# Kernel tuning notes

Hardware: AMD Instinct MI355X
Metric: run time of the kernel (lower is better)

Reference implementation:

```python
import jax, jax.numpy as jnp
import numpy as np

NUM_HEADS = 16
NUM_KV_HEADS = 8
HEAD_DIM = 128
GATE_LOW_RANK = 16
GATE_NORMALIZER = 16.0
NORM_EPS = 1e-5
CHUNK = 64


def gla_chunk(q, k, v, g, chunk=CHUNK):
    """Chunkwise-parallel gated linear attention.
    q,k,v,g: [B,H,L,D]. Recurrence: S_t = diag(exp(g_t)) S_{t-1} + k_t^T v_t; o_t = q_t S_t.
    """
    B, H, L, D = q.shape
    n = L // chunk

    def rs(x):  # -> [n, B, H, C, D]
        return x.reshape(B, H, n, chunk, D).transpose(2, 0, 1, 3, 4)

    qc, kc, vc, gc = rs(q), rs(k), rs(v), rs(g)
    causal = jnp.tril(jnp.ones((chunk, chunk), dtype=bool))

    def step(S, inp):
        qt, kt, vt, gt = inp                      # [B,H,C,D]
        b = jnp.cumsum(gt, axis=-2)               # inclusive cumulative log-gates
        q_ = qt * jnp.exp(b)
        k_ = kt * jnp.exp(-b)
        # intra-chunk causal attention (diag included)
        A = jnp.einsum('bhid,bhjd->bhij', q_, k_)
        A = jnp.where(causal, A, 0.0)
        o = jnp.einsum('bhij,bhje->bhie', A, vt)
        # inter-chunk contribution from carried state
        o = o + jnp.einsum('bhid,bhde->bhie', q_, S)
        # state update to end of chunk
        k_end = kt * jnp.exp(b[..., -1:, :] - b)
        S_new = S * jnp.exp(b[..., -1, :])[..., None] + jnp.einsum('bhcd,bhce->bhde', k_end, vt)
        return S_new, o

    S0 = jnp.zeros((B, H, D, D), q.dtype)
    _, o = jax.lax.scan(step, S0, (qc, kc, vc, gc))
    return o.transpose(1, 2, 0, 3, 4).reshape(B, H, L, D)


def setup_inputs() -> dict:
    key = jax.random.key(0)
    ks = jax.random.split(key, 10)
    B, L, HID = 2, 2048, 2048
    KV = NUM_KV_HEADS * HEAD_DIM  # 1024
    w = 0.02
    return {
        'hidden_states': jax.random.normal(ks[0], (B, L, HID), jnp.float32),
        'Wq': jax.random.normal(ks[1], (HID, HID), jnp.float32) * w,
        'bq': jnp.zeros((HID,), jnp.float32),
        'Wk': jax.random.normal(ks[2], (HID, KV), jnp.float32) * w,
        'bk': jnp.zeros((KV,), jnp.float32),
        'Wv': jax.random.normal(ks[3], (HID, KV), jnp.float32) * w,
        'bv': jnp.zeros((KV,), jnp.float32),
        'Wg1': jax.random.normal(ks[4], (HID, GATE_LOW_RANK), jnp.float32) * w,
        'Wg2': jax.random.normal(ks[5], (GATE_LOW_RANK, KV), jnp.float32) * w,
        'bg2': jnp.zeros((KV,), jnp.float32),
        'g_norm_w': jnp.ones((HEAD_DIM,), jnp.float32),
        'Wo': jax.random.normal(ks[6], (HID, HID), jnp.float32) * w,
    }


def reference(hidden_states, Wq, bq, Wk, bk, Wv, bv, Wg1, Wg2, bg2, g_norm_w, Wo):
    B, L, HID = hidden_states.shape
    H, HKV, D = NUM_HEADS, NUM_KV_HEADS, HEAD_DIM
    n_rep = H // HKV

    q = jax.nn.relu(hidden_states @ Wq + bq)          # feature_map = relu
    k = jax.nn.relu(hidden_states @ Wk + bk)
    v = hidden_states @ Wv + bv
    gk = jax.nn.log_sigmoid((hidden_states @ Wg1) @ Wg2 + bg2) / GATE_NORMALIZER

    q = q.reshape(B, L, H, D).transpose(0, 2, 1, 3)    # [B,H,L,D]
    def to_heads(x):
        return x.reshape(B, L, HKV, D).transpose(0, 2, 1, 3)
    k, v, gk = to_heads(k), to_heads(v), to_heads(gk)  # [B,HKV,L,D]
    # GQA: repeat kv heads
    k = jnp.repeat(k, n_rep, axis=1)
    v = jnp.repeat(v, n_rep, axis=1)
    gk = jnp.repeat(gk, n_rep, axis=1)

    q = q * (D ** -0.5)                                # scale as in chunk_gla
    o = gla_chunk(q, k, v, gk)                         # [B,H,L,D]

    # per-head RMSNorm over head_dim
    o = o * jax.lax.rsqrt(jnp.mean(o * o, axis=-1, keepdims=True) + NORM_EPS) * g_norm_w
    o = o.transpose(0, 2, 1, 3).reshape(B, L, H * D)
    return o @ Wo
```

## Files before the change

### kernel.cpp

```cpp
#include <hip/hip_runtime.h>

typedef unsigned short u16;
typedef u16 u16x8 __attribute__((ext_vector_type(8)));
typedef u16 u16x4 __attribute__((ext_vector_type(4)));
typedef __bf16 bf16x8 __attribute__((ext_vector_type(8)));
typedef float f32x4 __attribute__((ext_vector_type(4)));

#define DEVI static __device__ __forceinline__

DEVI float b2f(u16 u){ union { unsigned u; float f; } c; c.u = ((unsigned)u) << 16; return c.f; }
DEVI u16 f2b(float f){ union { float f; unsigned u; } c; c.f = f;
  unsigned r = c.u + 0x7fffu + ((c.u >> 16) & 1u); return (u16)(r >> 16); }
DEVI void gload16(const void* g, void* l){
  __builtin_amdgcn_global_load_lds((const __attribute__((address_space(1))) void*)g,
                                   (__attribute__((address_space(3))) void*)l, 16, 0, 0);
}
DEVI f32x4 MFMA(bf16x8 a, bf16x8 b, f32x4 c){
  return __builtin_amdgcn_mfma_f32_16x16x32_bf16(a, b, c, 0, 0, 0);
}
#define WAITV(n) asm volatile("s_waitcnt vmcnt(" #n ")" ::: "memory")
#define WAITL0()  asm volatile("s_waitcnt lgkmcnt(0)" ::: "memory")

constexpr size_t OFF_HB  = 0;
constexpr size_t OFF_WCT = OFF_HB  + (size_t)4096*2048*2;
constexpr size_t OFF_WOT = OFF_WCT + (size_t)4224*2048*2;
constexpr size_t OFF_QKV = OFF_WOT + (size_t)2048*2048*2;
constexpr size_t OFF_G1  = OFF_QKV + (size_t)4096*4096*2;
constexpr size_t OFF_G   = OFF_G1  + (size_t)4096*16*4;
constexpr size_t OFF_EB  = OFF_G   + (size_t)4096*1024*4;
constexpr size_t OFF_KD  = OFF_EB  + (size_t)4096*1024*2;
constexpr size_t OFF_T   = OFF_KD  + (size_t)4096*1024*2;
constexpr size_t OFF_DV  = OFF_T   + (size_t)2*8*32*128*128*2;
constexpr size_t OFF_SP  = OFF_DV  + (size_t)2*8*32*128*4;
constexpr size_t OFF_ON  = OFF_SP  + (size_t)2*8*32*128*128*2;

__global__ __launch_bounds__(256) void k_conv_h(const float* __restrict__ h, u16* __restrict__ hb){
  int idx = blockIdx.x*256 + threadIdx.x, stride = gridDim.x*256;
  for (int i = idx; i < 4096*2048/4; i += stride){
    float4 v = ((const float4*)h)[i];
    u16x4 o; o[0]=f2b(v.x); o[1]=f2b(v.y); o[2]=f2b(v.z); o[3]=f2b(v.w);
    ((u16x4*)hb)[i] = o;
  }
}

__global__ __launch_bounds__(256) void k_transpose(const float* __restrict__ src, u16* __restrict__ dst,
                                                   int K, int N, int rowOff, int pitch){
  __shared__ float tile[64][65];
  int kb = blockIdx.y*64, nb = blockIdx.x*64;
  int t = threadIdx.x, x = t & 63, y0 = t >> 6;
#pragma unroll
  for (int i = 0; i < 16; i++){
    int y = y0 + i*4, k = kb + y, n = nb + x;
    tile[y][x] = (n < N) ? src[(size_t)k*N + n] : 0.f;
  }
  __syncthreads();
#pragma unroll
  for (int i = 0; i < 16; i++){
    int y = y0 + i*4, n = nb + y, k = kb + x;
    if (n < N) dst[(size_t)(rowOff + n)*pitch + k] = f2b(tile[x][y]);
  }
}

template<int BM, int MODE>
__global__ __launch_bounds__(512, 2) void gemm256(const u16* __restrict__ A, const u16* __restrict__ Bt,
                                                  u16* __restrict__ Cq, float* __restrict__ Cf,
                                                  const float* __restrict__ bq, const float* __restrict__ bk,
                                                  const float* __restrict__ bv){
  constexpr int NT = 64;
  constexpr int MI = BM/32;
  constexpr int ALOADS = BM/128;
  constexpr int NTN = (MODE==0) ? 16 : 8;
  __shared__ u16 sA[4*BM*32];
  __shared__ u16 sB[4*256*32];
  int id = blockIdx.x;
  int swz = (id & 7)*32 + (id >> 3);
  int mt = swz / NTN, nt = swz % NTN;
  int t = threadIdx.x, w = t >> 6, l = t & 63;
  int wr = w >> 2, wc = w & 3;
  int mRow0 = mt*BM, nCol0 = nt*256;
  const u16* srcA[ALOADS]; const u16* srcB[2];
#pragma unroll
  for (int i = 0; i < ALOADS; i++){
    int S = t + i*512, r = S>>2, g = (S&3) ^ ((r>>2)&3);
    srcA[i] = A + (size_t)(mRow0 + r)*2048 + g*8;
  }
#pragma unroll
  for (int i = 0; i < 2; i++){
    int S = t + i*512, r = S>>2, g = (S&3) ^ ((r>>2)&3);
    srcB[i] = Bt + (size_t)(nCol0 + r)*2048 + g*8;
  }
  auto ISSUE = [&](int T){
    int buf = T & 3;
    u16* dA = sA + buf*(BM*32);
    u16* dB = sB + buf*(256*32);
#pragma unroll
    for (int i = 0; i < ALOADS; i++) gload16(srcA[i] + T*32, dA + (i*512 + w*64)*8);
#pragma unroll
    for (int i = 0; i < 2; i++)      gload16(srcB[i] + T*32, dB + (i*512 + w*64)*8);
  };
  f32x4 acc[MI][4] = {};
  ISSUE(0); ISSUE(1); ISSUE(2);
  for (int T = 0; T < NT; ++T){
    if (T + 3 < NT) ISSUE(T + 3);
    if constexpr (BM == 256){
      if (T < NT-3)       WAITV(12);
      else if (T == NT-3) WAITV(8);
      else if (T == NT-2) WAITV(4);
      else                WAITV(0);
    } else {
      if (T < NT-3)       WAITV(9);
      else if (T == NT-3) WAITV(6);
      else if (T == NT-2) WAITV(3);
      else                WAITV(0);
    }
    __builtin_amdgcn_s_barrier();
    const u16* bufA = sA + (T&3)*(BM*32);
    const u16* bufB = sB + (T&3)*(256*32);
    bf16x8 bfr[4], afr[MI];
#pragma unroll
    for (int ni = 0; ni < 4; ni++){
      int r = wc*64 + ni*16 + (l&15);
      int p = (l>>4) ^ ((r>>2)&3);
      bfr[ni] = *(const bf16x8*)&bufB[(r*4 + p)*8];
    }
#pragma unroll
    for (int mi = 0; mi < MI; mi++){
      int r = wr*(BM/2) + mi*16 + (l&15);
      int p = (l>>4) ^ ((r>>2)&3);
      afr[mi] = *(const bf16x8*)&bufA[(r*4 + p)*8];
    }
    __builtin_amdgcn_s_setprio(1);
#pragma unroll
    for (int mi = 0; mi < MI; mi++)
#pragma unroll
      for (int ni = 0; ni < 4; ni++)
        acc[mi][ni] = MFMA(afr[mi], bfr[ni], acc[mi][ni]);
    __builtin_amdgcn_s_setprio(0);
    WAITL0();
    __builtin_amdgcn_s_barrier();
  }
  int iLoc = (l>>4)*4, jc = l & 15;
  if (MODE == 0){
#pragma unroll
    for (int ni = 0; ni < 4; ni++){
      int n0 = nCol0 + wc*64 + ni*16;
      int n = n0 + jc;
      int kind; float bias;
      if (n0 < 2048){ kind = 0; bias = bq[n]; }
      else if (n0 < 3072){ kind = 1; bias = bk[n - 2048]; }
      else { kind = 2; bias = bv[n - 3072]; }
#pragma unroll
      for (int mi = 0; mi < MI; mi++){
        int m = mRow0 + wr*(BM/2) + mi*16 + iLoc;
#pragma unroll
        for (int rr = 0; rr < 4; rr++){
          float x = acc[mi][ni][rr] + bias;
          int row = m + rr;
          if (kind == 0)      Cq[(size_t)row*4096 + n] = f2b(fmaxf(x, 0.f) * 0.08838834764831845f);
          else if (kind == 1) Cq[(size_t)row*4096 + n] = f2b(fmaxf(x, 0.f));
          else                Cq[(size_t)row*4096 + n] = f2b(x);
        }
      }
    }
  } else {
#pragma unroll
    for (int ni = 0; ni < 4; ni++){
      int n = nCol0 + wc*64 + ni*16 + jc;
#pragma unroll
      for (int mi = 0; mi < MI; mi++){
        int m = mRow0 + wr*(BM/2) + mi*16 + iLoc;
#pragma unroll
        for (int rr = 0; rr < 4; rr++) Cf[(size_t)(m+rr)*2048 + n] = acc[mi][ni][rr];
      }
    }
  }
}

__global__ __launch_bounds__(256) void k_g1(const u16* __restrict__ hb, const float* __restrict__ Wg1,
                                            float* __restrict__ G1){
  int t = threadIdx.x;
  int tok = blockIdx.x*16 + (t>>4), j = t & 15;
  const u16* hr = hb + (size_t)tok*2048;
  float s = 0.f;
  for (int k = 0; k < 2048; k += 8){
    u16x8 hv = *(const u16x8*)&hr[k];
#pragma unroll
    for (int u = 0; u < 8; u++) s += b2f(hv[u]) * Wg1[(k+u)*16 + j];
  }
  G1[(size_t)tok*16 + j] = s;
}

__global__ __launch_bounds__(256) void k_gates(const float* __restrict__ G1, const float* __restrict__ Wg2,
                                               const float* __restrict__ bg2, float* __restrict__ g){
  __shared__ float w2[16*1024];
  __shared__ float bb[1024];
  __shared__ float g1l[256];
  int t = threadIdx.x;
  for (int i = t; i < 4096; i += 256) ((float4*)w2)[i] = ((const float4*)Wg2)[i];
  ((float4*)bb)[t] = ((const float4*)bg2)[t];
  int tok0 = blockIdx.x*16;
  g1l[t] = G1[(size_t)tok0*16 + t];
  __syncthreads();
  int c0 = t*4;
  for (int tk = 0; tk < 16; tk++){
    float4 a = *(const float4*)&bb[c0];
#pragma unroll
    for (int r = 0; r < 16; r++){
      float gv = g1l[tk*16 + r];
      float4 wr = *(const float4*)&w2[r*1024 + c0];
      a.x += gv*wr.x; a.y += gv*wr.y; a.z += gv*wr.z; a.w += gv*wr.w;
    }
    float4 o;
    o.x = (fminf(a.x,0.f) - log1pf(expf(-fabsf(a.x)))) * 0.0625f;
    o.y = (fminf(a.y,0.f) - log1pf(expf(-fabsf(a.y)))) * 0.0625f;
    o.z = (fminf(a.z,0.f) - log1pf(expf(-fabsf(a.z)))) * 0.0625f;
    o.w = (fminf(a.w,0.f) - log1pf(expf(-fabsf(a.w)))) * 0.0625f;
    *(float4*)&g[(size_t)(tok0+tk)*1024 + c0] = o;
  }
}

__global__ __launch_bounds__(256) void k_phaseA(const float* __restrict__ g, const u16* __restrict__ QKV,
                                                u16* __restrict__ eb, u16* __restrict__ kd,
                                                u16* __restrict__ T, float* __restrict__ Dv){
  __shared__ float gb[64*128];
  __shared__ u16 keT[128*72];
  __shared__ u16 vT [128*72];
  int c = blockIdx.x, kvh = blockIdx.y, b = blockIdx.z;
  int t = threadIdx.x;
  int tok0 = b*2048 + c*64;
#pragma unroll
  for (int r = 0; r < 8; r++){
    int idx4 = r*256 + t;
    int i = idx4 >> 5, c4 = idx4 & 31;
    ((float4*)gb)[i*32 + c4] = *(const float4*)&g[(size_t)(tok0+i)*1024 + kvh*128 + c4*4];
  }
  __syncthreads();
  if (t < 128){
    float run = 0.f;
    for (int i = 0; i < 64; i++){ run += gb[i*128 + t]; gb[i*128 + t] = run; }
    Dv[((size_t)(b*8+kvh)*32 + c)*128 + t] = expf(run);
  }
  __syncthreads();
  int d0 = (t&15)*8;
  float blast[8];
#pragma unroll
  for (int j = 0; j < 8; j++) blast[j] = gb[63*128 + d0 + j];
#pragma unroll
  for (int r = 0; r < 4; r++){
    int i = (t>>4) + r*16;
    u16x8 kv_ = *(const u16x8*)&QKV[(size_t)(tok0+i)*4096 + 2048 + kvh*128 + d0];
    u16x8 vv  = *(const u16x8*)&QKV[(size_t)(tok0+i)*4096 + 3072 + kvh*128 + d0];
    u16x8 ebv, kdv;
#pragma unroll
    for (int j = 0; j < 8; j++){
      float bcur = gb[i*128 + d0 + j];
      float kf = b2f(kv_[j]);
      ebv[j] = f2b(expf(bcur));
      kdv[j] = f2b(kf * expf(-bcur));
      keT[(d0+j)*72 + i] = f2b(kf * expf(blast[j] - bcur));
      vT [(d0+j)*72 + i] = vv[j];
    }
    *(u16x8*)&eb[(size_t)(tok0+i)*1024 + kvh*128 + d0] = ebv;
    *(u16x8*)&kd[(size_t)(tok0+i)*1024 + kvh*128 + d0] = kdv;
  }
  __syncthreads();
  int w = t>>6, l = t&63;
  f32x4 acc[2][8] = {};
#pragma unroll
  for (int ks = 0; ks < 2; ks++){
    bf16x8 af[2];
#pragma unroll
    for (int ti = 0; ti < 2; ti++)
      af[ti] = *(const bf16x8*)&keT[(w*32 + ti*16 + (l&15))*72 + ks*32 + (l>>4)*8];
#pragma unroll
    for (int tj = 0; tj < 8; tj++){
      bf16x8 bf_ = *(const bf16x8*)&vT[(tj*16 + (l&15))*72 + ks*32 + (l>>4)*8];
#pragma unroll
      for (int ti = 0; ti < 2; ti++) acc[ti][tj] = MFMA(af[ti], bf_, acc[ti][tj]);
    }
  }
  size_t tbase = ((size_t)(b*8+kvh)*32 + c)*16384;
#pragma unroll
  for (int ti = 0; ti < 2; ti++)
#pragma unroll
    for (int tj = 0; tj < 8; tj++)
#pragma unroll
      for (int rr = 0; rr < 4; rr++){
        int d = w*32 + ti*16 + (l>>4)*4 + rr, e = tj*16 + (l&15);
        T[tbase + d*128 + e] = f2b(acc[ti][tj][rr]);
      }
}

__global__ __launch_bounds__(256) void k_phaseB(const u16* __restrict__ T, const float* __restrict__ Dv,
                                                u16* __restrict__ SP){
  __shared__ u16 sl[16*128];
  int es = blockIdx.x, kvh = blockIdx.y, b = blockIdx.z;
  int t = threadIdx.x;
  size_t bh = (size_t)(b*8 + kvh);
  float S[8] = {0,0,0,0,0,0,0,0};
  for (int c = 0; c < 32; c++){
#pragma unroll
    for (int r = 0; r < 8; r++){
      int idx = r*256 + t, d = idx>>4, el = idx&15;
      sl[el*128 + d] = f2b(S[r]);
    }
    __syncthreads();
    size_t spb = (bh*32 + c)*16384 + (size_t)es*2048;
    *(u16x8*)&SP[spb + t*8] = *(const u16x8*)&sl[t*8];
    size_t tb  = (bh*32 + c)*16384;
    size_t dvb = (bh*32 + c)*128;
#pragma unroll
    for (int r = 0; r < 8; r++){
      int idx = r*256 + t, d = idx>>4, el = idx&15;
      float tv = b2f(T[tb + d*128 + es*16 + el]);
      S[r] = S[r]*Dv[dvb + d] + tv;
    }
    __syncthreads();
  }
}

__global__ __launch_bounds__(256) void k_phaseC(const u16* __restrict__ QKV, const u16* __restrict__ eb,
                                                const u16* __restrict__ kd, const u16* __restrict__ SP,
                                                const float* __restrict__ gnw, u16* __restrict__ onrm){
  __shared__ u16 kl[64*128];
  __shared__ u16 sl[64*72];
  __shared__ u16 vT[128*72];
  int c = blockIdx.x, h = blockIdx.y, b = blockIdx.z;
  int kvh = h >> 1;
  int t = threadIdx.x, w = t>>6, l = t&63;
  int tok0 = b*2048 + c*64;
#pragma unroll
  for (int is = 0; is < 4; is++){
    int row = (t>>4) + is*16;
    int d0s = 8*((t&15) ^ (row&7));
    gload16(&kd[(size_t)(tok0+row)*1024 + kvh*128 + d0s], &kl[is*2048 + w*512]);
  }
  int d0v = (t&15)*8;
#pragma unroll
  for (int r = 0; r < 4; r++){
    int i = (t>>4) + r*16;
    u16x8 vv = *(const u16x8*)&QKV[(size_t)(tok0+i)*4096 + 3072 + kvh*128 + d0v];
#pragma unroll
    for (int jj = 0; jj < 8; jj++) vT[(d0v+jj)*72 + i] = vv[jj];
  }
  bf16x8 aq[4];
  {
    int i = w*16 + (l&15);
#pragma unroll
    for (int kt = 0; kt < 4; kt++){
      int dq = kt*32 + (l>>4)*8;
      u16x8 qv = *(const u16x8*)&QKV[(size_t)(tok0+i)*4096 + h*128 + dq];
      u16x8 ev = *(const u16x8*)&eb[(size_t)(tok0+i)*1024 + kvh*128 + dq];
      u16x8 o;
#pragma unroll
      for (int jj = 0; jj < 8; jj++) o[jj] = f2b(b2f(qv[jj]) * b2f(ev[jj]));
      aq[kt] = __builtin_bit_cast(bf16x8, o);
    }
  }
  __syncthreads();
  f32x4 accs[4] = {};
#pragma unroll
  for (int kt = 0; kt < 4; kt++){
#pragma unroll
    for (int jt = 0; jt < 4; jt++){
      int j = jt*16 + (l&15);
      int byte_ = j*256 + ((2*(kt*32 + (l>>4)*8)) ^ ((j&7)<<4));
      bf16x8 bk_ = *(const bf16x8*)((const char*)kl + byte_);
      accs[jt] = MFMA(aq[kt], bk_, accs[jt]);
    }
  }
#pragma unroll
  for (int jt = 0; jt < 4; jt++)
#pragma unroll
    for (int rr = 0; rr < 4; rr++){
      int i = w*16 + (l>>4)*4 + rr;
      int j = jt*16 + (l&15);
      sl[i*72 + j] = f2b((i >= j) ? accs[jt][rr] : 0.f);
    }
  f32x4 acco[8] = {};
  size_t spb = ((size_t)(b*8+kvh)*32 + c)*16384;
#pragma unroll
  for (int kt = 0; kt < 4; kt++){
#pragma unroll
    for (int et = 0; et < 8; et++){
      int e = et*16 + (l&15);
      int dd = kt*32 + (l>>4)*8;
      bf16x8 bs = *(const bf16x8*)&SP[spb + (size_t)e*128 + dd];
      acco[et] = MFMA(aq[kt], bs, acco[et]);
    }
  }
#pragma unroll
  for (int kt2 = 0; kt2 < 2; kt2++){
    int i = w*16 + (l&15);
    bf16x8 as = *(const bf16x8*)&sl[i*72 + kt2*32 + (l>>4)*8];
#pragma unroll
    for (int et = 0; et < 8; et++){
      bf16x8 bv_ = *(const bf16x8*)&vT[(et*16 + (l&15))*72 + kt2*32 + (l>>4)*8];
      acco[et] = MFMA(as, bv_, acco[et]);
    }
  }
  float gw[8];
#pragma unroll
  for (int et = 0; et < 8; et++) gw[et] = gnw[et*16 + (l&15)];
#pragma unroll
  for (int rr = 0; rr < 4; rr++){
    int i = w*16 + (l>>4)*4 + rr;
    float ss = 0.f;
#pragma unroll
    for (int et = 0; et < 8; et++){ float x = acco[et][rr]; ss += x*x; }
    ss += __shfl_xor(ss, 1); ss += __shfl_xor(ss, 2);
    ss += __shfl_xor(ss, 4); ss += __shfl_xor(ss, 8);
    float sc = rsqrtf(ss*(1.f/128.f) + 1e-5f);
#pragma unroll
    for (int et = 0; et < 8; et++){
      int e = et*16 + (l&15);
      onrm[(size_t)(tok0+i)*2048 + h*128 + e] = f2b(acco[et][rr]*sc*gw[et]);
    }
  }
}

extern "C" void kernel_launch(void* const* d_in, const int* in_sizes, int n_in,
                              void* d_out, int out_size, void* d_ws, size_t ws_size,
                              hipStream_t stream){
  (void)in_sizes; (void)n_in; (void)out_size; (void)ws_size;
  const float* h   = (const float*)d_in[0];
  const float* Wq  = (const float*)d_in[1];
  const float* bq  = (const float*)d_in[2];
  const float* Wk  = (const float*)d_in[3];
  const float* bk  = (const float*)d_in[4];
  const float* Wv  = (const float*)d_in[5];
  const float* bv  = (const float*)d_in[6];
  const float* Wg1 = (const float*)d_in[7];
  const float* Wg2 = (const float*)d_in[8];
  const float* bg2 = (const float*)d_in[9];
  const float* gnw = (const float*)d_in[10];
  const float* Wo  = (const float*)d_in[11];
  float* out = (float*)d_out;
  char* ws = (char*)d_ws;
  u16*   hb   = (u16*)  (ws + OFF_HB);
  u16*   wct  = (u16*)  (ws + OFF_WCT);
  u16*   wot  = (u16*)  (ws + OFF_WOT);
  u16*   qkv  = (u16*)  (ws + OFF_QKV);
  float* g1   = (float*)(ws + OFF_G1);
  float* gbuf = (float*)(ws + OFF_G);
  u16*   ebuf = (u16*)  (ws + OFF_EB);
  u16*   kdb  = (u16*)  (ws + OFF_KD);
  u16*   Tb   = (u16*)  (ws + OFF_T);
  float* Dvb  = (float*)(ws + OFF_DV);
  u16*   SPb  = (u16*)  (ws + OFF_SP);
  u16*   onb  = (u16*)  (ws + OFF_ON);

  k_conv_h<<<2048, 256, 0, stream>>>(h, hb);
  k_transpose<<<dim3(32,32), 256, 0, stream>>>(Wq,  wct, 2048, 2048,    0, 2048);
  k_transpose<<<dim3(16,32), 256, 0, stream>>>(Wk,  wct, 2048, 1024, 2048, 2048);
  k_transpose<<<dim3(16,32), 256, 0, stream>>>(Wv,  wct, 2048, 1024, 3072, 2048);
  k_transpose<<<dim3(32,32), 256, 0, stream>>>(Wo,  wot, 2048, 2048,    0, 2048);
  gemm256<256,0><<<256, 512, 0, stream>>>(hb, wct, qkv, nullptr, bq, bk, bv);
  k_g1<<<256, 256, 0, stream>>>(hb, Wg1, g1);
  k_gates<<<256, 256, 0, stream>>>(g1, Wg2, bg2, gbuf);
  k_phaseA<<<dim3(32,8,2), 256, 0, stream>>>(gbuf, qkv, ebuf, kdb, Tb, Dvb);
  k_phaseB<<<dim3(8,8,2), 256, 0, stream>>>(Tb, Dvb, SPb);
  k_phaseC<<<dim3(32,16,2), 256, 0, stream>>>(qkv, ebuf, kdb, SPb, gnw, onb);
  gemm256<128,1><<<256, 512, 0, stream>>>(onb, wot, nullptr, out, nullptr, nullptr, nullptr);
}
```

Before: 503.1 us.

## Fold low-rank gate projection into QKV GEMM and restructure GEMM pipeline

Precomputes Wg1@Wg2 as a bf16 transposed weight so the gate logits come out of the main QKV GEMM as extra N columns. Log-sigmoid is applied in that GEMM's epilogue, which removes the separate k_g1 and k_gates kernels. The GEMM is also restructured to use 64-wide K steps with double buffering, an 8-way XOR swizzle, and MFMAs split into half-tiles interleaved with async LDS loads and barriers. The tradeoffs are higher gate FLOPs through the dense rank-2048 product, bf16 rounding of the combined gate weight, and more barriers per K step.

```diff
diff --git a/kernel.cpp b/kernel.cpp
--- a/kernel.cpp
+++ b/kernel.cpp
@@ -19,7 +19,7 @@
   return __builtin_amdgcn_mfma_f32_16x16x32_bf16(a, b, c, 0, 0, 0);
 }
 #define WAITV(n) asm volatile("s_waitcnt vmcnt(" #n ")" ::: "memory")
-#define WAITL0()  asm volatile("s_waitcnt lgkmcnt(0)" ::: "memory")
+#define BAR()    do { __builtin_amdgcn_s_barrier(); asm volatile("" ::: "memory"); } while(0)
 
 constexpr size_t OFF_HB  = 0;
 constexpr size_t OFF_WCT = OFF_HB  + (size_t)4096*2048*2;
@@ -61,83 +61,132 @@
   }
 }
 
+__global__ __launch_bounds__(256) void k_wtilde(const float* __restrict__ Wg1, const float* __restrict__ Wg2,
+                                                u16* __restrict__ wt){
+  int c = blockIdx.x, t = threadIdx.x;
+  float w2[16];
+#pragma unroll
+  for (int j = 0; j < 16; j++) w2[j] = Wg2[j*1024 + c];
+  int r0 = t*8;
+  u16x8 o;
+#pragma unroll
+  for (int u = 0; u < 8; u++){
+    const float* row = Wg1 + (size_t)(r0+u)*16;
+    float s = 0.f;
+#pragma unroll
+    for (int j = 0; j < 16; j++) s += row[j]*w2[j];
+    o[u] = f2b(s);
+  }
+  *(u16x8*)&wt[(size_t)c*2048 + r0] = o;
+}
+
 template<int BM, int MODE>
-__global__ __launch_bounds__(512, 2) void gemm256(const u16* __restrict__ A, const u16* __restrict__ Bt,
-                                                  u16* __restrict__ Cq, float* __restrict__ Cf,
-                                                  const float* __restrict__ bq, const float* __restrict__ bk,
-                                                  const float* __restrict__ bv){
-  constexpr int NT = 64;
+__global__ __launch_bounds__(512, 2) void gemm8p(const u16* __restrict__ A,
+                                                 const u16* __restrict__ BtLo,
+                                                 const u16* __restrict__ BtHi,
+                                                 u16* __restrict__ Cq, float* __restrict__ Cg,
+                                                 float* __restrict__ Cf,
+                                                 const float* __restrict__ bq,
+                                                 const float* __restrict__ bk,
+                                                 const float* __restrict__ bv,
+                                                 const float* __restrict__ bg2){
+  constexpr int K = 2048, NT = 32;
+  constexpr int FH = BM/64;
   constexpr int MI = BM/32;
-  constexpr int ALOADS = BM/128;
-  constexpr int NTN = (MODE==0) ? 16 : 8;
-  __shared__ u16 sA[4*BM*32];
-  __shared__ u16 sB[4*256*32];
+  constexpr int AL = BM*8/512;
+  constexpr int NTN = (MODE==0) ? 20 : 8;
+  constexpr int CPX = (MODE==0) ? 40 : 32;
+  __shared__ u16 sA[2*BM*64];
+  __shared__ u16 sB[2*256*64];
   int id = blockIdx.x;
-  int swz = (id & 7)*32 + (id >> 3);
+  int swz = (id & 7)*CPX + (id >> 3);
   int mt = swz / NTN, nt = swz % NTN;
   int t = threadIdx.x, w = t >> 6, l = t & 63;
   int wr = w >> 2, wc = w & 3;
   int mRow0 = mt*BM, nCol0 = nt*256;
-  const u16* srcA[ALOADS]; const u16* srcB[2];
-#pragma unroll
-  for (int i = 0; i < ALOADS; i++){
-    int S = t + i*512, r = S>>2, g = (S&3) ^ ((r>>2)&3);
-    srcA[i] = A + (size_t)(mRow0 + r)*2048 + g*8;
-  }
-#pragma unroll
-  for (int i = 0; i < 2; i++){
-    int S = t + i*512, r = S>>2, g = (S&3) ^ ((r>>2)&3);
-    srcB[i] = Bt + (size_t)(nCol0 + r)*2048 + g*8;
-  }
-  auto ISSUE = [&](int T){
-    int buf = T & 3;
-    u16* dA = sA + buf*(BM*32);
-    u16* dB = sB + buf*(256*32);
-#pragma unroll
-    for (int i = 0; i < ALOADS; i++) gload16(srcA[i] + T*32, dA + (i*512 + w*64)*8);
-#pragma unroll
-    for (int i = 0; i < 2; i++)      gload16(srcB[i] + T*32, dB + (i*512 + w*64)*8);
+  const u16* Bbase = (MODE==0 && nCol0 >= 4096) ? (BtHi + (size_t)(nCol0-4096)*K)
+                                                : (BtLo + (size_t)nCol0*K);
+  const u16* srcA[AL];
+#pragma unroll
+  for (int i = 0; i < AL; i++){
+    int G = i*512 + t, row = G>>3, g = (G&7) ^ (row&7);
+    srcA[i] = A + (size_t)(mRow0+row)*K + g*8;
+  }
+  const u16* srcB[2][2];
+#pragma unroll
+  for (int kk = 0; kk < 2; kk++)
+#pragma unroll
+    for (int i = 0; i < 2; i++){
+      int S = i*512 + t, row = S>>2, j = (S&3) ^ ((row>>1)&3);
+      srcB[kk][i] = Bbase + (size_t)row*K + kk*32 + j*8;
+    }
+  auto stA = [&](int T1, int i){
+    u16* d = sA + (T1&1)*(BM*64) + (size_t)(i*512 + w*64)*8;
+    gload16(srcA[i] + T1*64, d);
+  };
+  auto stB = [&](int T1, int kk, int i){
+    u16* d = sB + (T1&1)*(256*64) + kk*8192 + (size_t)(i*512 + w*64)*8;
+    gload16(srcB[kk][i] + T1*64, d);
+  };
+  bf16x8 af[FH], bfr[4];
+  auto rdA = [&](int slot, int mh, int kk){
+    const u16* base = sA + slot*(BM*64);
+#pragma unroll
+    for (int f = 0; f < FH; f++){
+      int row = wr*(BM/2) + mh*(BM/4) + f*16 + (l&15);
+      int gr = (kk*4 + (l>>4)) ^ (row&7);
+      af[f] = *(const bf16x8*)&base[row*64 + gr*8];
+    }
+  };
+  auto rdB = [&](int slot, int kk){
+    const u16* base = sB + slot*(256*64) + kk*8192;
+#pragma unroll
+    for (int n = 0; n < 4; n++){
+      int row = wc*64 + n*16 + (l&15);
+      int jr = (l>>4) ^ ((row>>1)&3);
+      bfr[n] = *(const bf16x8*)&base[row*32 + jr*8];
+    }
   };
   f32x4 acc[MI][4] = {};
-  ISSUE(0); ISSUE(1); ISSUE(2);
+  auto mm = [&](int mh){
+    __builtin_amdgcn_s_setprio(1);
+#pragma unroll
+    for (int f = 0; f < FH; f++)
+#pragma unroll
+      for (int n = 0; n < 4; n++)
+        acc[mh*FH+f][n] = MFMA(af[f], bfr[n], acc[mh*FH+f][n]);
+    __builtin_amdgcn_s_setprio(0);
+  };
+#pragma unroll
+  for (int i = 0; i < AL; i++) stA(0, i);
+  stB(0,0,0); stB(0,0,1); stB(0,1,0); stB(0,1,1);
+  WAITV(2);
+  BAR();
   for (int T = 0; T < NT; ++T){
-    if (T + 3 < NT) ISSUE(T + 3);
-    if constexpr (BM == 256){
-      if (T < NT-3)       WAITV(12);
-      else if (T == NT-3) WAITV(8);
-      else if (T == NT-2) WAITV(4);
-      else                WAITV(0);
-    } else {
-      if (T < NT-3)       WAITV(9);
-      else if (T == NT-3) WAITV(6);
-      else if (T == NT-2) WAITV(3);
-      else                WAITV(0);
-    }
-    __builtin_amdgcn_s_barrier();
-    const u16* bufA = sA + (T&3)*(BM*32);
-    const u16* bufB = sB + (T&3)*(256*32);
-    bf16x8 bfr[4], afr[MI];
-#pragma unroll
-    for (int ni = 0; ni < 4; ni++){
-      int r = wc*64 + ni*16 + (l&15);
-      int p = (l>>4) ^ ((r>>2)&3);
-      bfr[ni] = *(const bf16x8*)&bufB[(r*4 + p)*8];
-    }
-#pragma unroll
-    for (int mi = 0; mi < MI; mi++){
-      int r = wr*(BM/2) + mi*16 + (l&15);
-      int p = (l>>4) ^ ((r>>2)&3);
-      afr[mi] = *(const bf16x8*)&bufA[(r*4 + p)*8];
-    }
-    __builtin_amdgcn_s_setprio(1);
-#pragma unroll
-    for (int mi = 0; mi < MI; mi++)
-#pragma unroll
-      for (int ni = 0; ni < 4; ni++)
-        acc[mi][ni] = MFMA(afr[mi], bfr[ni], acc[mi][ni]);
-    __builtin_amdgcn_s_setprio(0);
-    WAITL0();
-    __builtin_amdgcn_s_barrier();
+    int slot = T & 1;
+    bool pf = (T+1 < NT);
+    rdA(slot, 0, 0); rdB(slot, 0);
+    if (pf){ stA(T+1,0); stA(T+1,1); }
+    BAR();
+    mm(0);
+    BAR();
+    rdA(slot, 1, 0);
+    if (pf){ if constexpr (BM==256){ stA(T+1,2); stA(T+1,3); } else { stB(T+1,0,0); stB(T+1,0,1); } }
+    BAR();
+    mm(1);
+    if (pf) WAITV(4); else WAITV(0);
+    BAR();
+    rdA(slot, 0, 1); rdB(slot, 1);
+    if (pf){ if constexpr (BM==256){ stB(T+1,0,0); stB(T+1,0,1); } else { stB(T+1,1,0); stB(T+1,1,1); } }
+    BAR();
+    mm(0);
+    BAR();
+    rdA(slot, 1, 1);
+    if (pf){ if constexpr (BM==256){ stB(T+1,1,0); stB(T+1,1,1); } }
+    BAR();
+    mm(1);
+    if (pf) WAITV(2);
+    BAR();
   }
   int iLoc = (l>>4)*4, jc = l & 15;
   if (MODE == 0){
@@ -148,17 +197,19 @@
       int kind; float bias;
       if (n0 < 2048){ kind = 0; bias = bq[n]; }
       else if (n0 < 3072){ kind = 1; bias = bk[n - 2048]; }
-      else { kind = 2; bias = bv[n - 3072]; }
+      else if (n0 < 4096){ kind = 2; bias = bv[n - 3072]; }
+      else { kind = 3; bias = bg2[n - 4096]; }
 #pragma unroll
       for (int mi = 0; mi < MI; mi++){
-        int m = mRow0 + wr*(BM/2) + mi*16 + iLoc;
+        int m = mRow0 + wr*(BM/2) + (mi/FH)*(BM/4) + (mi%FH)*16 + iLoc;
 #pragma unroll
         for (int rr = 0; rr < 4; rr++){
           float x = acc[mi][ni][rr] + bias;
           int row = m + rr;
           if (kind == 0)      Cq[(size_t)row*4096 + n] = f2b(fmaxf(x, 0.f) * 0.08838834764831845f);
           else if (kind == 1) Cq[(size_t)row*4096 + n] = f2b(fmaxf(x, 0.f));
-          else                Cq[(size_t)row*4096 + n] = f2b(x);
+          else if (kind == 2) Cq[(size_t)row*4096 + n] = f2b(x);
+          else Cg[(size_t)row*1024 + (n - 4096)] = (fminf(x,0.f) - log1pf(expf(-fabsf(x)))) * 0.0625f;
         }
       }
     }
@@ -168,54 +219,11 @@
       int n = nCol0 + wc*64 + ni*16 + jc;
 #pragma unroll
       for (int mi = 0; mi < MI; mi++){
-        int m = mRow0 + wr*(BM/2) + mi*16 + iLoc;
+        int m = mRow0 + wr*(BM/2) + (mi/FH)*(BM/4) + (mi%FH)*16 + iLoc;
 #pragma unroll
         for (int rr = 0; rr < 4; rr++) Cf[(size_t)(m+rr)*2048 + n] = acc[mi][ni][rr];
       }
     }
-  }
-}
-
-__global__ __launch_bounds__(256) void k_g1(const u16* __restrict__ hb, const float* __restrict__ Wg1,
-                                            float* __restrict__ G1){
-  int t = threadIdx.x;
-  int tok = blockIdx.x*16 + (t>>4), j = t & 15;
-  const u16* hr = hb + (size_t)tok*2048;
-  float s = 0.f;
-  for (int k = 0; k < 2048; k += 8){
-    u16x8 hv = *(const u16x8*)&hr[k];
-#pragma unroll
-    for (int u = 0; u < 8; u++) s += b2f(hv[u]) * Wg1[(k+u)*16 + j];
-  }
-  G1[(size_t)tok*16 + j] = s;
-}
-
-__global__ __launch_bounds__(256) void k_gates(const float* __restrict__ G1, const float* __restrict__ Wg2,
-                                               const float* __restrict__ bg2, float* __restrict__ g){
-  __shared__ float w2[16*1024];
-  __shared__ float bb[1024];
-  __shared__ float g1l[256];
-  int t = threadIdx.x;
-  for (int i = t; i < 4096; i += 256) ((float4*)w2)[i] = ((const float4*)Wg2)[i];
-  ((float4*)bb)[t] = ((const float4*)bg2)[t];
-  int tok0 = blockIdx.x*16;
-  g1l[t] = G1[(size_t)tok0*16 + t];
-  __syncthreads();
-  int c0 = t*4;
-  for (int tk = 0; tk < 16; tk++){
-    float4 a = *(const float4*)&bb[c0];
-#pragma unroll
-    for (int r = 0; r < 16; r++){
-      float gv = g1l[tk*16 + r];
-      float4 wr = *(const float4*)&w2[r*1024 + c0];
-      a.x += gv*wr.x; a.y += gv*wr.y; a.z += gv*wr.z; a.w += gv*wr.w;
-    }
-    float4 o;
-    o.x = (fminf(a.x,0.f) - log1pf(expf(-fabsf(a.x)))) * 0.0625f;
-    o.y = (fminf(a.y,0.f) - log1pf(expf(-fabsf(a.y)))) * 0.0625f;
-    o.z = (fminf(a.z,0.f) - log1pf(expf(-fabsf(a.z)))) * 0.0625f;
-    o.w = (fminf(a.w,0.f) - log1pf(expf(-fabsf(a.w)))) * 0.0625f;
-    *(float4*)&g[(size_t)(tok0+tk)*1024 + c0] = o;
   }
 }
 
@@ -441,11 +449,11 @@
   u16*   wct  = (u16*)  (ws + OFF_WCT);
   u16*   wot  = (u16*)  (ws + OFF_WOT);
   u16*   qkv  = (u16*)  (ws + OFF_QKV);
-  float* g1   = (float*)(ws + OFF_G1);
   float* gbuf = (float*)(ws + OFF_G);
   u16*   ebuf = (u16*)  (ws + OFF_EB);
   u16*   kdb  = (u16*)  (ws + OFF_KD);
   u16*   Tb   = (u16*)  (ws + OFF_T);
+  u16*   wtilT= (u16*)  (ws + OFF_T);
   float* Dvb  = (float*)(ws + OFF_DV);
   u16*   SPb  = (u16*)  (ws + OFF_SP);
   u16*   onb  = (u16*)  (ws + OFF_ON);
@@ -455,11 +463,10 @@
   k_transpose<<<dim3(16,32), 256, 0, stream>>>(Wk,  wct, 2048, 1024, 2048, 2048);
   k_transpose<<<dim3(16,32), 256, 0, stream>>>(Wv,  wct, 2048, 1024, 3072, 2048);
   k_transpose<<<dim3(32,32), 256, 0, stream>>>(Wo,  wot, 2048, 2048,    0, 2048);
-  gemm256<256,0><<<256, 512, 0, stream>>>(hb, wct, qkv, nullptr, bq, bk, bv);
-  k_g1<<<256, 256, 0, stream>>>(hb, Wg1, g1);
-  k_gates<<<256, 256, 0, stream>>>(g1, Wg2, bg2, gbuf);
+  k_wtilde<<<1024, 256, 0, stream>>>(Wg1, Wg2, wtilT);
+  gemm8p<256,0><<<320, 512, 0, stream>>>(hb, wct, wtilT, qkv, gbuf, nullptr, bq, bk, bv, bg2);
   k_phaseA<<<dim3(32,8,2), 256, 0, stream>>>(gbuf, qkv, ebuf, kdb, Tb, Dvb);
   k_phaseB<<<dim3(8,8,2), 256, 0, stream>>>(Tb, Dvb, SPb);
   k_phaseC<<<dim3(32,16,2), 256, 0, stream>>>(qkv, ebuf, kdb, SPb, gnw, onb);
-  gemm256<128,1><<<256, 512, 0, stream>>>(onb, wot, nullptr, out, nullptr, nullptr, nullptr);
-}
+  gemm8p<128,1><<<256, 512, 0, stream>>>(onb, wot, nullptr, nullptr, nullptr, out, nullptr, nullptr, nullptr, nullptr);
+}
```

New measurement: 649.4 us. 29.1% more time.

## Fold low-rank gate weights into dense matrix and compute gates via MFMA GEMM

Applied to the files above, without the earlier changes.

Precomputes Wg1@Wg2 as a bf16 2048x1024 transposed weight, then computes gate logits with an MFMA GEMM over the bf16 hidden states instead of the scalar k_g1 and k_gates kernels. The log-sigmoid is moved into phaseA's gate load. The LDS swizzle in the GEMMs also changes from (r>>2)&3 to (r>>1)&3 to reduce bank conflicts. This trades the rank-16 factorization for a full 4096x1024x2048 GEMM of extra FLOPs, and the bf16 rounding of the combined weight may shift gate accuracy.

```diff
diff --git a/kernel.cpp b/kernel.cpp
--- a/kernel.cpp
+++ b/kernel.cpp
@@ -19,7 +19,7 @@
   return __builtin_amdgcn_mfma_f32_16x16x32_bf16(a, b, c, 0, 0, 0);
 }
 #define WAITV(n) asm volatile("s_waitcnt vmcnt(" #n ")" ::: "memory")
-#define WAITL0()  asm volatile("s_waitcnt lgkmcnt(0)" ::: "memory")
+#define WAITL0() asm volatile("s_waitcnt lgkmcnt(0)" ::: "memory")
 
 constexpr size_t OFF_HB  = 0;
 constexpr size_t OFF_WCT = OFF_HB  + (size_t)4096*2048*2;
@@ -58,6 +58,36 @@
   for (int i = 0; i < 16; i++){
     int y = y0 + i*4, n = nb + y, k = kb + x;
     if (n < N) dst[(size_t)(rowOff + n)*pitch + k] = f2b(tile[x][y]);
+  }
+}
+
+__global__ __launch_bounds__(256) void k_wtilde(const float* __restrict__ Wg1, const float* __restrict__ Wg2,
+                                                u16* __restrict__ wt){
+  __shared__ float w2s[16*8];
+  int c0 = blockIdx.x*8, t = threadIdx.x;
+  if (t < 128){ int j = t>>3, cc = t&7; w2s[j*8+cc] = Wg2[j*1024 + c0 + cc]; }
+  __syncthreads();
+  int r0 = t*8;
+#pragma unroll
+  for (int half = 0; half < 2; half++){
+    float rowv[4][16];
+#pragma unroll
+    for (int u = 0; u < 4; u++)
+#pragma unroll
+      for (int j4 = 0; j4 < 4; j4++)
+        *(float4*)&rowv[u][j4*4] = *(const float4*)&Wg1[(size_t)(r0 + half*4 + u)*16 + j4*4];
+#pragma unroll
+    for (int cc = 0; cc < 8; cc++){
+      u16x4 o;
+#pragma unroll
+      for (int u = 0; u < 4; u++){
+        float s = 0.f;
+#pragma unroll
+        for (int j = 0; j < 16; j++) s += rowv[u][j]*w2s[j*8+cc];
+        o[u] = f2b(s);
+      }
+      *(u16x4*)&wt[(size_t)(c0+cc)*2048 + r0 + half*4] = o;
+    }
   }
 }
 
@@ -81,12 +111,12 @@
   const u16* srcA[ALOADS]; const u16* srcB[2];
 #pragma unroll
   for (int i = 0; i < ALOADS; i++){
-    int S = t + i*512, r = S>>2, g = (S&3) ^ ((r>>2)&3);
+    int S = t + i*512, r = S>>2, g = (S&3) ^ ((r>>1)&3);
     srcA[i] = A + (size_t)(mRow0 + r)*2048 + g*8;
   }
 #pragma unroll
   for (int i = 0; i < 2; i++){
-    int S = t + i*512, r = S>>2, g = (S&3) ^ ((r>>2)&3);
+    int S = t + i*512, r = S>>2, g = (S&3) ^ ((r>>1)&3);
     srcB[i] = Bt + (size_t)(nCol0 + r)*2048 + g*8;
   }
   auto ISSUE = [&](int T){
@@ -120,13 +150,13 @@
 #pragma unroll
     for (int ni = 0; ni < 4; ni++){
       int r = wc*64 + ni*16 + (l&15);
-      int p = (l>>4) ^ ((r>>2)&3);
+      int p = (l>>4) ^ ((r>>1)&3);
       bfr[ni] = *(const bf16x8*)&bufB[(r*4 + p)*8];
     }
 #pragma unroll
     for (int mi = 0; mi < MI; mi++){
       int r = wr*(BM/2) + mi*16 + (l&15);
-      int p = (l>>4) ^ ((r>>2)&3);
+      int p = (l>>4) ^ ((r>>1)&3);
       afr[mi] = *(const bf16x8*)&bufA[(r*4 + p)*8];
     }
     __builtin_amdgcn_s_setprio(1);
@@ -176,46 +206,78 @@
   }
 }
 
-__global__ __launch_bounds__(256) void k_g1(const u16* __restrict__ hb, const float* __restrict__ Wg1,
-                                            float* __restrict__ G1){
-  int t = threadIdx.x;
-  int tok = blockIdx.x*16 + (t>>4), j = t & 15;
-  const u16* hr = hb + (size_t)tok*2048;
-  float s = 0.f;
-  for (int k = 0; k < 2048; k += 8){
-    u16x8 hv = *(const u16x8*)&hr[k];
-#pragma unroll
-    for (int u = 0; u < 8; u++) s += b2f(hv[u]) * Wg1[(k+u)*16 + j];
-  }
-  G1[(size_t)tok*16 + j] = s;
-}
-
-__global__ __launch_bounds__(256) void k_gates(const float* __restrict__ G1, const float* __restrict__ Wg2,
-                                               const float* __restrict__ bg2, float* __restrict__ g){
-  __shared__ float w2[16*1024];
-  __shared__ float bb[1024];
-  __shared__ float g1l[256];
-  int t = threadIdx.x;
-  for (int i = t; i < 4096; i += 256) ((float4*)w2)[i] = ((const float4*)Wg2)[i];
-  ((float4*)bb)[t] = ((const float4*)bg2)[t];
-  int tok0 = blockIdx.x*16;
-  g1l[t] = G1[(size_t)tok0*16 + t];
-  __syncthreads();
-  int c0 = t*4;
-  for (int tk = 0; tk < 16; tk++){
-    float4 a = *(const float4*)&bb[c0];
-#pragma unroll
-    for (int r = 0; r < 16; r++){
-      float gv = g1l[tk*16 + r];
-      float4 wr = *(const float4*)&w2[r*1024 + c0];
-      a.x += gv*wr.x; a.y += gv*wr.y; a.z += gv*wr.z; a.w += gv*wr.w;
-    }
-    float4 o;
-    o.x = (fminf(a.x,0.f) - log1pf(expf(-fabsf(a.x)))) * 0.0625f;
-    o.y = (fminf(a.y,0.f) - log1pf(expf(-fabsf(a.y)))) * 0.0625f;
-    o.z = (fminf(a.z,0.f) - log1pf(expf(-fabsf(a.z)))) * 0.0625f;
-    o.w = (fminf(a.w,0.f) - log1pf(expf(-fabsf(a.w)))) * 0.0625f;
-    *(float4*)&g[(size_t)(tok0+tk)*1024 + c0] = o;
+__global__ __launch_bounds__(256, 2) void gemmG(const u16* __restrict__ A, const u16* __restrict__ Bt,
+                                                float* __restrict__ Cg, const float* __restrict__ bg2){
+  constexpr int NT = 64;
+  __shared__ u16 sA[4*128*32];
+  __shared__ u16 sB[4*128*32];
+  int id = blockIdx.x;
+  int swz = (id & 7)*32 + (id >> 3);
+  int mt = swz >> 3, nt = swz & 7;
+  int t = threadIdx.x, w = t >> 6, l = t & 63;
+  int wr = w >> 1, wc = w & 1;
+  int mRow0 = mt*128, nCol0 = nt*128;
+  const u16* srcA[2]; const u16* srcB[2];
+#pragma unroll
+  for (int i = 0; i < 2; i++){
+    int S = t + i*256, r = S>>2, g = (S&3) ^ ((r>>1)&3);
+    srcA[i] = A + (size_t)(mRow0 + r)*2048 + g*8;
+    srcB[i] = Bt + (size_t)(nCol0 + r)*2048 + g*8;
+  }
+  auto ISSUE = [&](int T){
+    int buf = T & 3;
+    u16* dA = sA + buf*4096;
+    u16* dB = sB + buf*4096;
+#pragma unroll
+    for (int i = 0; i < 2; i++) gload16(srcA[i] + T*32, dA + (i*256 + w*64)*8);
+#pragma unroll
+    for (int i = 0; i < 2; i++) gload16(srcB[i] + T*32, dB + (i*256 + w*64)*8);
+  };
+  f32x4 acc[4][4] = {};
+  ISSUE(0); ISSUE(1); ISSUE(2);
+  for (int T = 0; T < NT; ++T){
+    if (T + 3 < NT) ISSUE(T + 3);
+    if (T < NT-3)       WAITV(12);
+    else if (T == NT-3) WAITV(8);
+    else if (T == NT-2) WAITV(4);
+    else                WAITV(0);
+    __builtin_amdgcn_s_barrier();
+    const u16* bufA = sA + (T&3)*4096;
+    const u16* bufB = sB + (T&3)*4096;
+    bf16x8 bfr[4], afr[4];
+#pragma unroll
+    for (int ni = 0; ni < 4; ni++){
+      int r = wc*64 + ni*16 + (l&15);
+      int p = (l>>4) ^ ((r>>1)&3);
+      bfr[ni] = *(const bf16x8*)&bufB[(r*4 + p)*8];
+    }
+#pragma unroll
+    for (int mi = 0; mi < 4; mi++){
+      int r = wr*64 + mi*16 + (l&15);
+      int p = (l>>4) ^ ((r>>1)&3);
+      afr[mi] = *(const bf16x8*)&bufA[(r*4 + p)*8];
+    }
+    __builtin_amdgcn_s_setprio(1);
+#pragma unroll
+    for (int mi = 0; mi < 4; mi++)
+#pragma unroll
+      for (int ni = 0; ni < 4; ni++)
+        acc[mi][ni] = MFMA(afr[mi], bfr[ni], acc[mi][ni]);
+    __builtin_amdgcn_s_setprio(0);
+    WAITL0();
+    __builtin_amdgcn_s_barrier();
+  }
+  int iLoc = (l>>4)*4, jc = l & 15;
+#pragma unroll
+  for (int ni = 0; ni < 4; ni++){
+    int n = nCol0 + wc*64 + ni*16 + jc;
+    float bias = bg2[n];
+#pragma unroll
+    for (int mi = 0; mi < 4; mi++){
+      int m = mRow0 + wr*64 + mi*16 + iLoc;
+#pragma unroll
+      for (int rr = 0; rr < 4; rr++) Cg[(size_t)(m+rr)*1024 + n] = acc[mi][ni][rr] + bias;
+    }
   }
 }
 
@@ -232,7 +294,13 @@
   for (int r = 0; r < 8; r++){
     int idx4 = r*256 + t;
     int i = idx4 >> 5, c4 = idx4 & 31;
-    ((float4*)gb)[i*32 + c4] = *(const float4*)&g[(size_t)(tok0+i)*1024 + kvh*128 + c4*4];
+    float4 v = *(const float4*)&g[(size_t)(tok0+i)*1024 + kvh*128 + c4*4];
+    float4 o;
+    o.x = (fminf(v.x,0.f) - log1pf(expf(-fabsf(v.x)))) * 0.0625f;
+    o.y = (fminf(v.y,0.f) - log1pf(expf(-fabsf(v.y)))) * 0.0625f;
+    o.z = (fminf(v.z,0.f) - log1pf(expf(-fabsf(v.z)))) * 0.0625f;
+    o.w = (fminf(v.w,0.f) - log1pf(expf(-fabsf(v.w)))) * 0.0625f;
+    ((float4*)gb)[i*32 + c4] = o;
   }
   __syncthreads();
   if (t < 128){
@@ -441,11 +509,11 @@
   u16*   wct  = (u16*)  (ws + OFF_WCT);
   u16*   wot  = (u16*)  (ws + OFF_WOT);
   u16*   qkv  = (u16*)  (ws + OFF_QKV);
-  float* g1   = (float*)(ws + OFF_G1);
   float* gbuf = (float*)(ws + OFF_G);
   u16*   ebuf = (u16*)  (ws + OFF_EB);
   u16*   kdb  = (u16*)  (ws + OFF_KD);
   u16*   Tb   = (u16*)  (ws + OFF_T);
+  u16*   wtilT= (u16*)  (ws + OFF_T);
   float* Dvb  = (float*)(ws + OFF_DV);
   u16*   SPb  = (u16*)  (ws + OFF_SP);
   u16*   onb  = (u16*)  (ws + OFF_ON);
@@ -455,9 +523,9 @@
   k_transpose<<<dim3(16,32), 256, 0, stream>>>(Wk,  wct, 2048, 1024, 2048, 2048);
   k_transpose<<<dim3(16,32), 256, 0, stream>>>(Wv,  wct, 2048, 1024, 3072, 2048);
   k_transpose<<<dim3(32,32), 256, 0, stream>>>(Wo,  wot, 2048, 2048,    0, 2048);
+  k_wtilde<<<128, 256, 0, stream>>>(Wg1, Wg2, wtilT);
   gemm256<256,0><<<256, 512, 0, stream>>>(hb, wct, qkv, nullptr, bq, bk, bv);
-  k_g1<<<256, 256, 0, stream>>>(hb, Wg1, g1);
-  k_gates<<<256, 256, 0, stream>>>(g1, Wg2, bg2, gbuf);
+  gemmG<<<256, 256, 0, stream>>>(hb, wtilT, gbuf, bg2);
   k_phaseA<<<dim3(32,8,2), 256, 0, stream>>>(gbuf, qkv, ebuf, kdb, Tb, Dvb);
   k_phaseB<<<dim3(8,8,2), 256, 0, stream>>>(Tb, Dvb, SPb);
   k_phaseC<<<dim3(32,16,2), 256, 0, stream>>>(qkv, ebuf, kdb, SPb, gnw, onb);
```

Measured after the change: 475.8 us. -5.4%, faster.
